# Kernel tuning notes

Hardware: AMD Instinct MI355X
Metric: run time of the kernel (lower is better)

Reference implementation:

```python
import jax, jax.numpy as jnp
import numpy as np

N = 50000      # nodes (batched molecular graphs)
E = 800000     # edges
G = 2048       # graphs in the batch
IN = 128       # in_channels
H = 128        # hidden
EPS = 1e-5     # BatchNorm eps


def _glorot(key, shape):
    lim = float(np.sqrt(6.0 / (shape[0] + shape[1])))
    return jax.random.uniform(key, shape, jnp.float32, -lim, lim)


def setup_inputs() -> dict:
    key = jax.random.key(0)
    ks = jax.random.split(key, 8)
    x = jax.random.normal(ks[0], (N, IN), jnp.float32)
    edge_index = jax.random.randint(ks[1], (2, E), 0, N, dtype=jnp.int64)
    batch = jnp.sort(jax.random.randint(ks[2], (N,), 0, G, dtype=jnp.int64))
    return {
        "x": x,
        "edge_index": edge_index,
        "batch": batch,
        "W1": _glorot(ks[3], (IN, H)), "b1": jnp.zeros((H,), jnp.float32),
        "gamma1": jnp.ones((H,), jnp.float32), "beta1": jnp.zeros((H,), jnp.float32),
        "W2": _glorot(ks[4], (H, H)), "b2": jnp.zeros((H,), jnp.float32),
        "gamma2": jnp.ones((H,), jnp.float32), "beta2": jnp.zeros((H,), jnp.float32),
        "Wout": _glorot(ks[5], (H, 1)), "bout": jnp.zeros((1,), jnp.float32),
    }


def gcn_conv(x, src, dst, W, b):
    # PyG GCNConv: add self-loops, symmetric norm D^-1/2 (A+I) D^-1/2, transform-first.
    n = x.shape[0]
    loop = jnp.arange(n, dtype=src.dtype)
    s = jnp.concatenate([src, loop])           # [E+N]
    d = jnp.concatenate([dst, loop])
    deg = jax.ops.segment_sum(jnp.ones_like(d, jnp.float32), d, num_segments=n)
    dinv = jnp.where(deg > 0, jax.lax.rsqrt(deg), 0.0)
    norm = dinv[s] * dinv[d]                   # [E+N]
    xw = x @ W                                 # [N, H] transform first (cheaper)
    msg = xw[s] * norm[:, None]                # [E+N, H] gathered, normalized messages
    out = jax.ops.segment_sum(msg, d, num_segments=n)  # scatter-add aggregate
    return out + b


def batch_norm(x, gamma, beta):
    # BatchNorm1d training-mode forward: batch stats, biased variance.
    mean = jnp.mean(x, axis=0)
    var = jnp.mean(jnp.square(x - mean), axis=0)
    return (x - mean) * jax.lax.rsqrt(var + EPS) * gamma + beta


def reference(x, edge_index, batch, W1, b1, gamma1, beta1, W2, b2, gamma2, beta2, Wout, bout):
    src, dst = edge_index[0], edge_index[1]
    h = jax.nn.relu(batch_norm(gcn_conv(x, src, dst, W1, b1), gamma1, beta1))
    h = jax.nn.relu(batch_norm(gcn_conv(h, src, dst, W2, b2), gamma2, beta2))
    # global_mean_pool over graph ids
    sums = jax.ops.segment_sum(h, batch, num_segments=G)            # [G, H]
    cnts = jax.ops.segment_sum(jnp.ones((h.shape[0],), h.dtype), batch, num_segments=G)
    pooled = sums / jnp.maximum(cnts, 1.0)[:, None]
    return pooled @ Wout + bout                                     # [G, 1]
```

## Files before the change

### kernel.cpp

```cpp
#include <hip/hip_runtime.h>
#include <stdint.h>

#define HD 128
#define EPS 1e-5f
#define NPB 256
#define SENT 0xFFFFFFFFu

typedef __attribute__((ext_vector_type(8))) short bf16x8;
typedef __attribute__((ext_vector_type(4))) float f32x4;

__device__ inline unsigned bf_round(float f) {
  unsigned u = __float_as_uint(f);
  return (u + 0x7fffu + ((u >> 16) & 1u)) >> 16;
}
__device__ inline unsigned bf_pack2(float x, float y) {
  return bf_round(x) | (bf_round(y) << 16);
}
__device__ inline float2 bf_unpack2(unsigned u) {
  float2 r;
  r.x = __uint_as_float(u << 16);
  r.y = __uint_as_float(u & 0xffff0000u);
  return r;
}

__global__ void k_prep(const float* __restrict__ W1, const float* __restrict__ W2,
                       unsigned short* __restrict__ Wt1, unsigned short* __restrict__ Wt2,
                       int* __restrict__ bline, float* __restrict__ sums1,
                       float* __restrict__ sums2, int nbline) {
  int b = blockIdx.x, t = threadIdx.x;
  if (b < 64) {
    int e = b * 256 + t;
    int k = e >> 7, c = e & 127;
    Wt1[c * 128 + k] = (unsigned short)bf_round(W1[e]);
  } else if (b < 128) {
    int e = (b - 64) * 256 + t;
    int k = e >> 7, c = e & 127;
    Wt2[c * 128 + k] = (unsigned short)bf_round(W2[e]);
  } else {
    int i = (b - 128) * 256 + t;
    if (i < nbline) bline[i] = 0;
    if (i < 256) { sums1[i] = 0.f; sums2[i] = 0.f; }
  }
}

__global__ __launch_bounds__(256) void k_phaseA(const int* __restrict__ src, const int* __restrict__ dst,
                                                int* __restrict__ bline, unsigned* __restrict__ arena,
                                                int E, int NBKT, int capLines, int chunk) {
  __shared__ int hist[NPB], gbase[NPB], ccap[NPB], lpos[NPB];
  const int t = threadIdx.x;
  for (int i = t; i < NPB; i += 256) { hist[i] = 0; lpos[i] = 0; }
  __syncthreads();
  const int e0 = blockIdx.x * chunk;
  const int e1 = (e0 + chunk < E) ? e0 + chunk : E;
  for (int i = e0 + t; i < e1; i += 256) atomicAdd(&hist[dst[i] >> 8], 1);
  __syncthreads();
  for (int b = t; b < NBKT; b += 256) {
    int n = hist[b];
    int nl = (n + 15) >> 4;
    int base = nl ? atomicAdd(&bline[b * 16], nl) : 0;
    if (base + nl > capLines) nl = (base < capLines) ? capLines - base : 0;
    gbase[b] = b * capLines * 16 + base * 16;
    ccap[b] = nl * 16;
  }
  __syncthreads();
  for (int i = e0 + t; i < e1; i += 256) {
    int d = dst[i];
    int b = d >> 8;
    int lp = atomicAdd(&lpos[b], 1);
    if (lp < ccap[b]) arena[gbase[b] + lp] = ((unsigned)src[i] << 8) | (unsigned)(d & 255);
  }
  __syncthreads();
  for (int b = t; b < NBKT; b += 256) {
    int n = lpos[b] < ccap[b] ? lpos[b] : ccap[b];
    for (int j = n; j < ccap[b]; ++j) arena[gbase[b] + j] = SENT;
  }
}

__global__ __launch_bounds__(256) void k_phaseB(const unsigned* __restrict__ arena,
                                                const int* __restrict__ bline,
                                                unsigned short* __restrict__ colidx,
                                                unsigned* __restrict__ nodeinfo,
                                                float* __restrict__ dinv,
                                                int N, int capLines) {
  __shared__ int deg[NPB], pos[NPB], scan[NPB];
  const int b = blockIdx.x;
  const int t = threadIdx.x;
  deg[t] = 0;
  __syncthreads();
  int used = bline[b * 16];
  if (used > capLines) used = capLines;
  const int slots = used * 16;
  const unsigned* seg = arena + (size_t)b * capLines * 16;
  for (int s = t; s < slots; s += 256) {
    unsigned u = seg[s];
    if (u != SENT) atomicAdd(&deg[u & 255], 1);
  }
  __syncthreads();
  int v = deg[t];
  scan[t] = v;
  __syncthreads();
  for (int off = 1; off < 256; off <<= 1) {
    int tv = (t >= off) ? scan[t - off] : 0;
    __syncthreads();
    scan[t] += tv;
    __syncthreads();
  }
  int prefix = scan[t] - v;
  pos[t] = prefix;
  int n = b * NPB + t;
  if (n < N) {
    unsigned off = (unsigned)(b * capLines * 16 + prefix);
    unsigned d8 = (unsigned)(v < 255 ? v : 255);
    nodeinfo[n] = (off << 8) | d8;
    dinv[n] = rsqrtf((float)v + 1.0f);
  }
  __syncthreads();
  unsigned short* cseg = colidx + (size_t)b * capLines * 16;
  for (int s = t; s < slots; s += 256) {
    unsigned u = seg[s];
    if (u != SENT) {
      int p = atomicAdd(&pos[u & 255], 1);
      cseg[p] = (unsigned short)(u >> 8);
    }
  }
}

#define SAB_LD 136
__global__ __launch_bounds__(256) void k_gemm(const float* __restrict__ Af32,
                                              const unsigned* __restrict__ Abf,
                                              const unsigned short* __restrict__ Wt,
                                              unsigned* __restrict__ Yp, int N,
                                              const float* __restrict__ dinv,
                                              const float* __restrict__ sums,
                                              const float* __restrict__ gamma,
                                              const float* __restrict__ beta, float invN) {
  __shared__ unsigned short sWt[128 * SAB_LD];
  __shared__ unsigned short sAb[64 * SAB_LD];
  __shared__ float sSc[128], sSh[128];
  const int tid = threadIdx.x;
  const int row0 = blockIdx.x * 64;
  for (int i = tid * 8; i < 128 * 128; i += 256 * 8) {
    int c = i >> 7, k = i & 127;
    uint4 v = *(const uint4*)&Wt[i];
    *(uint4*)&sWt[c * SAB_LD + k] = v;
  }
  if (sums && tid < 128) {
    float mean = sums[tid] * invN;
    float var = sums[128 + tid] * invN - mean * mean;
    float sc = gamma[tid] * rsqrtf(var + EPS);
    sSc[tid] = sc;
    sSh[tid] = beta[tid] - mean * sc;
  }
  __syncthreads();
  for (int i = tid * 4; i < 64 * 128; i += 256 * 4) {
    int r = i >> 7, c = i & 127;
    int gr = row0 + r;
    float4 v = make_float4(0.f, 0.f, 0.f, 0.f);
    if (gr < N) {
      if (Abf) {
        uint2 u = *(const uint2*)&Abf[(size_t)gr * 64 + (c >> 1)];
        float2 a = bf_unpack2(u.x), bq = bf_unpack2(u.y);
        v = make_float4(a.x, a.y, bq.x, bq.y);
      } else {
        v = *(const float4*)&Af32[(size_t)gr * HD + c];
      }
    }
    if (sums) {
      v.x = fmaxf(0.f, v.x * sSc[c + 0] + sSh[c + 0]);
      v.y = fmaxf(0.f, v.y * sSc[c + 1] + sSh[c + 1]);
      v.z = fmaxf(0.f, v.z * sSc[c + 2] + sSh[c + 2]);
      v.w = fmaxf(0.f, v.w * sSc[c + 3] + sSh[c + 3]);
    }
    unsigned lo = bf_round(v.x) | (bf_round(v.y) << 16);
    unsigned hi = bf_round(v.z) | (bf_round(v.w) << 16);
    *(uint2*)&sAb[r * SAB_LD + c] = make_uint2(lo, hi);
  }
  __syncthreads();
  const int w = tid >> 6;
  const int l = tid & 63;
  const int lr = l & 15;
  const int lk = (l >> 4) * 8;
  const unsigned short* aRow = &sAb[(w * 16 + lr) * SAB_LD];
  f32x4 acc[8];
#pragma unroll
  for (int t = 0; t < 8; ++t) acc[t] = (f32x4){0.f, 0.f, 0.f, 0.f};
#pragma unroll
  for (int kk = 0; kk < 128; kk += 32) {
    bf16x8 af = *(const bf16x8*)&aRow[kk + lk];
#pragma unroll
    for (int t = 0; t < 8; ++t) {
      bf16x8 bfr = *(const bf16x8*)&sWt[(t * 16 + lr) * SAB_LD + kk + lk];
      acc[t] = __builtin_amdgcn_mfma_f32_16x16x32_bf16(af, bfr, acc[t], 0, 0, 0);
    }
  }
  const int rbase = row0 + w * 16 + (l >> 4) * 4;
#pragma unroll
  for (int j = 0; j < 4; ++j) {
    int r = rbase + j;
    float d = (r < N) ? dinv[r] : 0.f;
#pragma unroll
    for (int t = 0; t < 8; ++t) {
      float v = acc[t][j] * d;
      float vn = __shfl_xor(v, 1, 64);
      if ((lr & 1) == 0 && r < N) {
        Yp[(size_t)r * 64 + t * 8 + (lr >> 1)] = bf_round(v) | (bf_round(vn) << 16);
      }
    }
  }
}

__global__ __launch_bounds__(256) void k_aggregate(const unsigned* __restrict__ Yp,
                                                   const unsigned* __restrict__ nodeinfo,
                                                   const unsigned short* __restrict__ colidx,
                                                   const float* __restrict__ dinv,
                                                   unsigned* __restrict__ Out, int N) {
  int n = (blockIdx.x * blockDim.x + threadIdx.x) >> 6;
  int lane = threadIdx.x & 63;
  if (n >= N) return;
  const unsigned info = nodeinfo[n];
  const int beg = (int)(info >> 8);
  const int deg = (int)(info & 255);
  const int m = deg < 64 ? deg : 64;
  int nbr = (lane < deg) ? (int)colidx[beg + lane] : 0;
  float2 self = bf_unpack2(Yp[(size_t)n * 64 + lane]);
  float ax = self.x, ay = self.y;
  int j = 0;
  for (; j + 8 <= m; j += 8) {
    unsigned u0 = Yp[(size_t)__shfl(nbr, j + 0, 64) * 64 + lane];
    unsigned u1 = Yp[(size_t)__shfl(nbr, j + 1, 64) * 64 + lane];
    unsigned u2 = Yp[(size_t)__shfl(nbr, j + 2, 64) * 64 + lane];
    unsigned u3 = Yp[(size_t)__shfl(nbr, j + 3, 64) * 64 + lane];
    unsigned u4 = Yp[(size_t)__shfl(nbr, j + 4, 64) * 64 + lane];
    unsigned u5 = Yp[(size_t)__shfl(nbr, j + 5, 64) * 64 + lane];
    unsigned u6 = Yp[(size_t)__shfl(nbr, j + 6, 64) * 64 + lane];
    unsigned u7 = Yp[(size_t)__shfl(nbr, j + 7, 64) * 64 + lane];
    float2 v0 = bf_unpack2(u0), v1 = bf_unpack2(u1), v2 = bf_unpack2(u2), v3 = bf_unpack2(u3);
    float2 v4 = bf_unpack2(u4), v5 = bf_unpack2(u5), v6 = bf_unpack2(u6), v7 = bf_unpack2(u7);
    ax += ((v0.x + v1.x) + (v2.x + v3.x)) + ((v4.x + v5.x) + (v6.x + v7.x));
    ay += ((v0.y + v1.y) + (v2.y + v3.y)) + ((v4.y + v5.y) + (v6.y + v7.y));
  }
  for (; j < m; ++j) {
    float2 v0 = bf_unpack2(Yp[(size_t)__shfl(nbr, j, 64) * 64 + lane]);
    ax += v0.x; ay += v0.y;
  }
  for (int e = beg + 64; e < beg + deg; ++e) {
    float2 v0 = bf_unpack2(Yp[(size_t)colidx[e] * 64 + lane]);
    ax += v0.x; ay += v0.y;
  }
  float dd = dinv[n];
  Out[(size_t)n * 64 + lane] = bf_pack2(ax * dd, ay * dd);
}

__global__ __launch_bounds__(256) void k_colstats(const unsigned* __restrict__ X, int N,
                                                  float* __restrict__ sums) {
  const int c2 = threadIdx.x & 63;
  const int half = threadIdx.x >> 6;
  float sx = 0.f, sy = 0.f, qx = 0.f, qy = 0.f;
  for (int r = blockIdx.x * 4 + half; r < N; r += gridDim.x * 4) {
    float2 v = bf_unpack2(X[(size_t)r * 64 + c2]);
    sx += v.x; sy += v.y; qx += v.x * v.x; qy += v.y * v.y;
  }
  __shared__ float l0[256], l1[256], l2[256], l3[256];
  l0[threadIdx.x] = sx; l1[threadIdx.x] = sy; l2[threadIdx.x] = qx; l3[threadIdx.x] = qy;
  __syncthreads();
  if (threadIdx.x < 64) {
    int t = threadIdx.x;
    sx = l0[t] + l0[t + 64] + l0[t + 128] + l0[t + 192];
    sy = l1[t] + l1[t + 64] + l1[t + 128] + l1[t + 192];
    qx = l2[t] + l2[t + 64] + l2[t + 128] + l2[t + 192];
    qy = l3[t] + l3[t + 64] + l3[t + 128] + l3[t + 192];
    int c = t * 2;
    atomicAdd(&sums[c], sx);
    atomicAdd(&sums[c + 1], sy);
    atomicAdd(&sums[128 + c], qx);
    atomicAdd(&sums[129 + c], qy);
  }
}

__global__ __launch_bounds__(256) void k_finalnode(const unsigned* __restrict__ Agg,
                                                   const float* __restrict__ sums,
                                                   const float* __restrict__ gamma,
                                                   const float* __restrict__ beta,
                                                   const float* __restrict__ wout,
                                                   float* __restrict__ nodescalar,
                                                   int N, float invN) {
  int n = (blockIdx.x * blockDim.x + threadIdx.x) >> 6;
  int lane = threadIdx.x & 63;
  if (n >= N) return;
  int c = lane * 2;
  float mean0 = sums[c] * invN;
  float var0 = sums[128 + c] * invN - mean0 * mean0;
  float sc0 = gamma[c] * rsqrtf(var0 + EPS);
  float sh0 = beta[c] - mean0 * sc0;
  float mean1 = sums[c + 1] * invN;
  float var1 = sums[129 + c] * invN - mean1 * mean1;
  float sc1 = gamma[c + 1] * rsqrtf(var1 + EPS);
  float sh1 = beta[c + 1] - mean1 * sc1;
  float2 v = bf_unpack2(Agg[(size_t)n * 64 + lane]);
  float h0 = fmaxf(0.f, v.x * sc0 + sh0);
  float h1 = fmaxf(0.f, v.y * sc1 + sh1);
  float p = h0 * wout[c] + h1 * wout[c + 1];
  for (int off = 32; off > 0; off >>= 1) p += __shfl_down(p, off);
  if (lane == 0) nodescalar[n] = p;
}

__global__ void k_finalout(const float* __restrict__ nodescalar, const int* __restrict__ batch,
                           const float* __restrict__ bout, float* __restrict__ out,
                           int G, int N) {
  int g = blockIdx.x * blockDim.x + threadIdx.x;
  if (g >= G) return;
  int lo = 0, hi = N;
  while (lo < hi) { int mid = (lo + hi) >> 1; if (batch[mid] < g) lo = mid + 1; else hi = mid; }
  int lb = lo;
  hi = N;
  while (lo < hi) { int mid = (lo + hi) >> 1; if (batch[mid] <= g) lo = mid + 1; else hi = mid; }
  float s = 0.f;
  for (int i = lb; i < lo; ++i) s += nodescalar[i];
  float cnt = (float)(lo - lb);
  out[g] = s / fmaxf(cnt, 1.0f) + bout[0];
}

extern "C" void kernel_launch(void* const* d_in, const int* in_sizes, int n_in,
                              void* d_out, int out_size, void* d_ws, size_t ws_size,
                              hipStream_t stream) {
  (void)n_in; (void)ws_size;
  const float* x      = (const float*)d_in[0];
  const int*   ei     = (const int*)d_in[1];
  const int*   batch  = (const int*)d_in[2];
  const float* W1     = (const float*)d_in[3];
  const float* gamma1 = (const float*)d_in[5];
  const float* beta1  = (const float*)d_in[6];
  const float* W2     = (const float*)d_in[7];
  const float* gamma2 = (const float*)d_in[9];
  const float* beta2  = (const float*)d_in[10];
  const float* wout   = (const float*)d_in[11];
  const float* bout   = (const float*)d_in[12];
  float* out = (float*)d_out;

  const int N = in_sizes[0] / HD;
  const int E = in_sizes[1] / 2;
  const int G = out_size;
  const int* src = ei;
  const int* dst = ei + E;
  const int NBKT = (N + NPB - 1) / NPB;
  const int NWGA = 256;
  const int chunk = (E + NWGA - 1) / NWGA;
  const int capLines = E / (NBKT * 16) + NWGA + 64;
  const int capSlots = capLines * 16;
  const float invN = 1.0f / (float)N;

  char* p = (char*)d_ws;
  auto carve = [&](size_t bytes) { char* r = p; p += (bytes + 255) & ~(size_t)255; return r; };
  unsigned* bufY = (unsigned*)carve((size_t)N * 64 * 4);
  unsigned* bufAgg = (unsigned*)carve((size_t)N * 64 * 4);
  unsigned* arena = (unsigned*)carve((size_t)NBKT * capSlots * 4);
  unsigned short* colidx = (unsigned short*)carve((size_t)NBKT * capSlots * 2);
  unsigned short* Wt1 = (unsigned short*)carve(128 * 128 * 2);
  unsigned short* Wt2 = (unsigned short*)carve(128 * 128 * 2);
  unsigned* nodeinfo = (unsigned*)carve((size_t)N * 4);
  float* dinv    = (float*)carve((size_t)N * 4);
  float* nodescalar = (float*)carve((size_t)N * 4);
  int*   bline = (int*)carve((size_t)NBKT * 16 * 4);
  float* sums1 = (float*)carve(256 * 4);
  float* sums2 = (float*)carve(256 * 4);

  const int nbline = NBKT * 16;
  const int pblocks = 128 + (nbline + 255) / 256;
  k_prep<<<pblocks, 256, 0, stream>>>(W1, W2, Wt1, Wt2, bline, sums1, sums2, nbline);

  k_phaseA<<<NWGA, 256, 0, stream>>>(src, dst, bline, arena, E, NBKT, capLines, chunk);
  k_phaseB<<<NBKT, 256, 0, stream>>>(arena, bline, colidx, nodeinfo, dinv, N, capLines);

  int gblocks = (N + 63) / 64;
  int ablocks = (N + 3) / 4;
  k_gemm<<<gblocks, 256, 0, stream>>>(x, nullptr, Wt1, bufY, N, dinv, nullptr, nullptr, nullptr, invN);
  k_aggregate<<<ablocks, 256, 0, stream>>>(bufY, nodeinfo, colidx, dinv, bufAgg, N);
  k_colstats<<<512, 256, 0, stream>>>(bufAgg, N, sums1);
  k_gemm<<<gblocks, 256, 0, stream>>>(nullptr, bufAgg, Wt2, bufY, N, dinv, sums1, gamma1, beta1, invN);
  k_aggregate<<<ablocks, 256, 0, stream>>>(bufY, nodeinfo, colidx, dinv, bufAgg, N);
  k_colstats<<<512, 256, 0, stream>>>(bufAgg, N, sums2);
  k_finalnode<<<ablocks, 256, 0, stream>>>(bufAgg, sums2, gamma2, beta2, wout, nodescalar, N, invN);
  k_finalout<<<(G + 255) / 256, 256, 0, stream>>>(nodescalar, batch, bout, out, G, N);
}
```

Baseline: 233.6 us.

## Split feature buffers into two column halves to shrink gather working set

```diff
diff --git a/kernel.cpp b/kernel.cpp
--- a/kernel.cpp
+++ b/kernel.cpp
@@ -127,10 +127,11 @@
 
 #define SAB_LD 136
 __global__ __launch_bounds__(256) void k_gemm(const float* __restrict__ Af32,
-                                              const unsigned* __restrict__ Abf,
+                                              const unsigned* __restrict__ AbfA,
+                                              const unsigned* __restrict__ AbfB,
                                               const unsigned short* __restrict__ Wt,
-                                              unsigned* __restrict__ Yp, int N,
-                                              const float* __restrict__ dinv,
+                                              unsigned* __restrict__ YA, unsigned* __restrict__ YB,
+                                              int N, const float* __restrict__ dinv,
                                               const float* __restrict__ sums,
                                               const float* __restrict__ gamma,
                                               const float* __restrict__ beta, float invN) {
@@ -157,8 +158,10 @@
     int gr = row0 + r;
     float4 v = make_float4(0.f, 0.f, 0.f, 0.f);
     if (gr < N) {
-      if (Abf) {
-        uint2 u = *(const uint2*)&Abf[(size_t)gr * 64 + (c >> 1)];
+      if (AbfA) {
+        const unsigned* H = (c < 64) ? AbfA : AbfB;
+        int cc = c & 63;
+        uint2 u = *(const uint2*)&H[(size_t)gr * 32 + (cc >> 1)];
         float2 a = bf_unpack2(u.x), bq = bf_unpack2(u.y);
         v = make_float4(a.x, a.y, bq.x, bq.y);
       } else {
@@ -203,61 +206,73 @@
       float v = acc[t][j] * d;
       float vn = __shfl_xor(v, 1, 64);
       if ((lr & 1) == 0 && r < N) {
-        Yp[(size_t)r * 64 + t * 8 + (lr >> 1)] = bf_round(v) | (bf_round(vn) << 16);
+        unsigned pv = bf_round(v) | (bf_round(vn) << 16);
+        if (t < 4) YA[(size_t)r * 32 + t * 8 + (lr >> 1)] = pv;
+        else       YB[(size_t)r * 32 + (t - 4) * 8 + (lr >> 1)] = pv;
       }
     }
   }
 }
 
-__global__ __launch_bounds__(256) void k_aggregate(const unsigned* __restrict__ Yp,
+__global__ __launch_bounds__(256) void k_aggregate(const unsigned* __restrict__ YA,
+                                                   const unsigned* __restrict__ YB,
                                                    const unsigned* __restrict__ nodeinfo,
                                                    const unsigned short* __restrict__ colidx,
                                                    const float* __restrict__ dinv,
-                                                   unsigned* __restrict__ Out, int N) {
-  int n = (blockIdx.x * blockDim.x + threadIdx.x) >> 6;
-  int lane = threadIdx.x & 63;
-  if (n >= N) return;
-  const unsigned info = nodeinfo[n];
+                                                   unsigned* __restrict__ OutA,
+                                                   unsigned* __restrict__ OutB,
+                                                   int N, int halfBlocks) {
+  int bid = blockIdx.x;
+  const unsigned* Y;
+  unsigned* O;
+  if (bid < halfBlocks) { Y = YA; O = OutA; }
+  else { Y = YB; O = OutB; bid -= halfBlocks; }
+  int g = (bid * 256 + threadIdx.x) >> 5;
+  if (g >= N) return;
+  const int sl = threadIdx.x & 31;
+  const int hb = threadIdx.x & 32;
+  const unsigned info = nodeinfo[g];
   const int beg = (int)(info >> 8);
   const int deg = (int)(info & 255);
-  const int m = deg < 64 ? deg : 64;
-  int nbr = (lane < deg) ? (int)colidx[beg + lane] : 0;
-  float2 self = bf_unpack2(Yp[(size_t)n * 64 + lane]);
-  float ax = self.x, ay = self.y;
-  int j = 0;
-  for (; j + 8 <= m; j += 8) {
-    unsigned u0 = Yp[(size_t)__shfl(nbr, j + 0, 64) * 64 + lane];
-    unsigned u1 = Yp[(size_t)__shfl(nbr, j + 1, 64) * 64 + lane];
-    unsigned u2 = Yp[(size_t)__shfl(nbr, j + 2, 64) * 64 + lane];
-    unsigned u3 = Yp[(size_t)__shfl(nbr, j + 3, 64) * 64 + lane];
-    unsigned u4 = Yp[(size_t)__shfl(nbr, j + 4, 64) * 64 + lane];
-    unsigned u5 = Yp[(size_t)__shfl(nbr, j + 5, 64) * 64 + lane];
-    unsigned u6 = Yp[(size_t)__shfl(nbr, j + 6, 64) * 64 + lane];
-    unsigned u7 = Yp[(size_t)__shfl(nbr, j + 7, 64) * 64 + lane];
-    float2 v0 = bf_unpack2(u0), v1 = bf_unpack2(u1), v2 = bf_unpack2(u2), v3 = bf_unpack2(u3);
-    float2 v4 = bf_unpack2(u4), v5 = bf_unpack2(u5), v6 = bf_unpack2(u6), v7 = bf_unpack2(u7);
-    ax += ((v0.x + v1.x) + (v2.x + v3.x)) + ((v4.x + v5.x) + (v6.x + v7.x));
-    ay += ((v0.y + v1.y) + (v2.y + v3.y)) + ((v4.y + v5.y) + (v6.y + v7.y));
-  }
-  for (; j < m; ++j) {
-    float2 v0 = bf_unpack2(Yp[(size_t)__shfl(nbr, j, 64) * 64 + lane]);
-    ax += v0.x; ay += v0.y;
-  }
-  for (int e = beg + 64; e < beg + deg; ++e) {
-    float2 v0 = bf_unpack2(Yp[(size_t)colidx[e] * 64 + lane]);
-    ax += v0.x; ay += v0.y;
-  }
-  float dd = dinv[n];
-  Out[(size_t)n * 64 + lane] = bf_pack2(ax * dd, ay * dd);
-}
-
-__global__ __launch_bounds__(256) void k_colstats(const unsigned* __restrict__ X, int N,
+  float2 s = bf_unpack2(Y[(size_t)g * 32 + sl]);
+  float ax = s.x, ay = s.y;
+  for (int base = 0; base < deg; base += 32) {
+    int cnt = deg - base; if (cnt > 32) cnt = 32;
+    int nbr = (sl < cnt) ? (int)colidx[beg + base + sl] : 0;
+    int j = 0;
+    for (; j + 8 <= cnt; j += 8) {
+      unsigned u0 = Y[(size_t)__shfl(nbr, hb + j + 0, 64) * 32 + sl];
+      unsigned u1 = Y[(size_t)__shfl(nbr, hb + j + 1, 64) * 32 + sl];
+      unsigned u2 = Y[(size_t)__shfl(nbr, hb + j + 2, 64) * 32 + sl];
+      unsigned u3 = Y[(size_t)__shfl(nbr, hb + j + 3, 64) * 32 + sl];
+      unsigned u4 = Y[(size_t)__shfl(nbr, hb + j + 4, 64) * 32 + sl];
+      unsigned u5 = Y[(size_t)__shfl(nbr, hb + j + 5, 64) * 32 + sl];
+      unsigned u6 = Y[(size_t)__shfl(nbr, hb + j + 6, 64) * 32 + sl];
+      unsigned u7 = Y[(size_t)__shfl(nbr, hb + j + 7, 64) * 32 + sl];
+      float2 v0 = bf_unpack2(u0), v1 = bf_unpack2(u1), v2 = bf_unpack2(u2), v3 = bf_unpack2(u3);
+      float2 v4 = bf_unpack2(u4), v5 = bf_unpack2(u5), v6 = bf_unpack2(u6), v7 = bf_unpack2(u7);
+      ax += ((v0.x + v1.x) + (v2.x + v3.x)) + ((v4.x + v5.x) + (v6.x + v7.x));
+      ay += ((v0.y + v1.y) + (v2.y + v3.y)) + ((v4.y + v5.y) + (v6.y + v7.y));
+    }
+    for (; j < cnt; ++j) {
+      float2 v0 = bf_unpack2(Y[(size_t)__shfl(nbr, hb + j, 64) * 32 + sl]);
+      ax += v0.x; ay += v0.y;
+    }
+  }
+  float dd = dinv[g];
+  O[(size_t)g * 32 + sl] = bf_pack2(ax * dd, ay * dd);
+}
+
+__global__ __launch_bounds__(256) void k_colstats(const unsigned* __restrict__ XA,
+                                                  const unsigned* __restrict__ XB, int N,
                                                   float* __restrict__ sums) {
   const int c2 = threadIdx.x & 63;
   const int half = threadIdx.x >> 6;
+  const unsigned* H = (c2 < 32) ? XA : XB;
+  const int idx = c2 & 31;
   float sx = 0.f, sy = 0.f, qx = 0.f, qy = 0.f;
   for (int r = blockIdx.x * 4 + half; r < N; r += gridDim.x * 4) {
-    float2 v = bf_unpack2(X[(size_t)r * 64 + c2]);
+    float2 v = bf_unpack2(H[(size_t)r * 32 + idx]);
     sx += v.x; sy += v.y; qx += v.x * v.x; qy += v.y * v.y;
   }
   __shared__ float l0[256], l1[256], l2[256], l3[256];
@@ -277,7 +292,8 @@
   }
 }
 
-__global__ __launch_bounds__(256) void k_finalnode(const unsigned* __restrict__ Agg,
+__global__ __launch_bounds__(256) void k_finalnode(const unsigned* __restrict__ AggA,
+                                                   const unsigned* __restrict__ AggB,
                                                    const float* __restrict__ sums,
                                                    const float* __restrict__ gamma,
                                                    const float* __restrict__ beta,
@@ -296,7 +312,8 @@
   float var1 = sums[129 + c] * invN - mean1 * mean1;
   float sc1 = gamma[c + 1] * rsqrtf(var1 + EPS);
   float sh1 = beta[c + 1] - mean1 * sc1;
-  float2 v = bf_unpack2(Agg[(size_t)n * 64 + lane]);
+  const unsigned* H = (lane < 32) ? AggA : AggB;
+  float2 v = bf_unpack2(H[(size_t)n * 32 + (lane & 31)]);
   float h0 = fmaxf(0.f, v.x * sc0 + sh0);
   float h1 = fmaxf(0.f, v.y * sc1 + sh1);
   float p = h0 * wout[c] + h1 * wout[c + 1];
@@ -351,8 +368,10 @@
 
   char* p = (char*)d_ws;
   auto carve = [&](size_t bytes) { char* r = p; p += (bytes + 255) & ~(size_t)255; return r; };
-  unsigned* bufY = (unsigned*)carve((size_t)N * 64 * 4);
-  unsigned* bufAgg = (unsigned*)carve((size_t)N * 64 * 4);
+  unsigned* YA = (unsigned*)carve((size_t)N * 32 * 4);
+  unsigned* YB = (unsigned*)carve((size_t)N * 32 * 4);
+  unsigned* AggA = (unsigned*)carve((size_t)N * 32 * 4);
+  unsigned* AggB = (unsigned*)carve((size_t)N * 32 * 4);
   unsigned* arena = (unsigned*)carve((size_t)NBKT * capSlots * 4);
   unsigned short* colidx = (unsigned short*)carve((size_t)NBKT * capSlots * 2);
   unsigned short* Wt1 = (unsigned short*)carve(128 * 128 * 2);
@@ -371,14 +390,18 @@
   k_phaseA<<<NWGA, 256, 0, stream>>>(src, dst, bline, arena, E, NBKT, capLines, chunk);
   k_phaseB<<<NBKT, 256, 0, stream>>>(arena, bline, colidx, nodeinfo, dinv, N, capLines);
 
-  int gblocks = (N + 63) / 64;
-  int ablocks = (N + 3) / 4;
-  k_gemm<<<gblocks, 256, 0, stream>>>(x, nullptr, Wt1, bufY, N, dinv, nullptr, nullptr, nullptr, invN);
-  k_aggregate<<<ablocks, 256, 0, stream>>>(bufY, nodeinfo, colidx, dinv, bufAgg, N);
-  k_colstats<<<512, 256, 0, stream>>>(bufAgg, N, sums1);
-  k_gemm<<<gblocks, 256, 0, stream>>>(nullptr, bufAgg, Wt2, bufY, N, dinv, sums1, gamma1, beta1, invN);
-  k_aggregate<<<ablocks, 256, 0, stream>>>(bufY, nodeinfo, colidx, dinv, bufAgg, N);
-  k_colstats<<<512, 256, 0, stream>>>(bufAgg, N, sums2);
-  k_finalnode<<<ablocks, 256, 0, stream>>>(bufAgg, sums2, gamma2, beta2, wout, nodescalar, N, invN);
+  const int gblocks = (N + 63) / 64;
+  const int halfBlocks = (N * 32 + 255) / 256;
+  const int ablocks = 2 * halfBlocks;
+  const int fblocks = (N * 64 + 255) / 256;
+  k_gemm<<<gblocks, 256, 0, stream>>>(x, nullptr, nullptr, Wt1, YA, YB, N, dinv,
+                                      nullptr, nullptr, nullptr, invN);
+  k_aggregate<<<ablocks, 256, 0, stream>>>(YA, YB, nodeinfo, colidx, dinv, AggA, AggB, N, halfBlocks);
+  k_colstats<<<512, 256, 0, stream>>>(AggA, AggB, N, sums1);
+  k_gemm<<<gblocks, 256, 0, stream>>>(nullptr, AggA, AggB, Wt2, YA, YB, N, dinv,
+                                      sums1, gamma1, beta1, invN);
+  k_aggregate<<<ablocks, 256, 0, stream>>>(YA, YB, nodeinfo, colidx, dinv, AggA, AggB, N, halfBlocks);
+  k_colstats<<<512, 256, 0, stream>>>(AggA, AggB, N, sums2);
+  k_finalnode<<<fblocks, 256, 0, stream>>>(AggA, AggB, sums2, gamma2, beta2, wout, nodescalar, N, invN);
   k_finalout<<<(G + 255) / 256, 256, 0, stream>>>(nodescalar, batch, bout, out, G, N);
 }
```

Result: no change. 238.2 us (+2.0%).
